# Kernel optimization log

Measured on AMD Instinct MI355X. Metric: run time of the kernel, lower is better.

The kernel has to match this reference:

```python
import jax, jax.numpy as jnp
import numpy as np

K = 30  # top-k spatial positions kept per channel


def setup_inputs() -> dict:
    key = jax.random.key(0)
    k1, k2, k3 = jax.random.split(key, 3)
    b, c, h, w = 32, 384, 56, 56
    x = jax.random.normal(k1, (b, c, h, w), dtype=jnp.float32)
    # depthwise conv: torch weight shape (C, 1, 3, 3), bias (C,)
    fan_in = 1 * 3 * 3
    bound = 1.0 / np.sqrt(fan_in)
    weight = jax.random.uniform(k2, (c, 1, 3, 3), dtype=jnp.float32, minval=-bound, maxval=bound)
    bias = jax.random.uniform(k3, (c,), dtype=jnp.float32, minval=-bound, maxval=bound)
    return {"x": x, "weight": weight, "bias": bias}


def reference(x, weight, bias):
    b, c, h, w = x.shape
    # depthwise 3x3 conv, padding=1 (SAME), groups=c
    scores = jax.lax.conv_general_dilated(
        x, weight,
        window_strides=(1, 1),
        padding="SAME",
        feature_group_count=c,
        dimension_numbers=("NCHW", "OIHW", "NCHW"),
    ) + bias[None, :, None, None]
    scores_flat = scores.reshape(b, c, h * w)
    _, topk_idx = jax.lax.top_k(scores_flat, K)  # (b, c, K)
    bi = jnp.arange(b)[:, None, None]
    ci = jnp.arange(c)[None, :, None]
    mask = jnp.zeros((b, c, h * w), dtype=x.dtype).at[bi, ci, topk_idx].set(1.0)
    return x * mask.reshape(b, c, h, w)
```

## Files before the change

### kernel.cpp

```cpp
#include <hip/hip_runtime.h>

#define NT 256
#define W 56
#define HW 3136
#define PW 60
#define GUARD 64
#define PAD_SZ (GUARD + 58*PW)
#define KSEL 30
#define NQ (HW/4)
#define CAP 160
#define ACT 196

typedef float v2f __attribute__((ext_vector_type(2)));

__device__ __forceinline__ v2f vfma(v2f a, v2f b, v2f c) {
#if __has_builtin(__builtin_elementwise_fma)
    return __builtin_elementwise_fma(a, b, c);
#else
    v2f r; r.x = fmaf(a.x, b.x, c.x); r.y = fmaf(a.y, b.y, c.y); return r;
#endif
}

__global__ __launch_bounds__(NT, 8) void topk_spatial_kernel(
    const float* __restrict__ x,
    const float* __restrict__ wgt,
    const float* __restrict__ bias,
    float* __restrict__ out,
    int C)
{
    __shared__ float        xs[PAD_SZ];
    __shared__ unsigned int smax[NT];
    __shared__ int          c_idx[CAP];
    __shared__ double       c_sd[CAP];
    __shared__ unsigned int keepw[HW / 32];
    __shared__ unsigned int s_T16;
    __shared__ int s_cnt;

    const int tid = threadIdx.x;
    const int bc  = blockIdx.x;
    const int ci  = bc % C;

    const float* xp = x   + (size_t)bc * HW;
    float*       op = out + (size_t)bc * HW;

    const float* wpt = wgt + (size_t)ci * 9;
    const float wk[3][3] = { { wpt[0], wpt[1], wpt[2] },
                             { wpt[3], wpt[4], wpt[5] },
                             { wpt[6], wpt[7], wpt[8] } };
    const float bv = bias[ci];

    if (tid < GUARD) xs[tid] = 0.0f;
    if (tid < PW) {
        xs[GUARD + tid] = 0.0f;
        xs[GUARD + 57 * PW + tid] = 0.0f;
    }
    if (tid < 224) {
        const int rr = 1 + (tid >> 2);
        xs[GUARD + rr * PW + 56 + (tid & 3)] = 0.0f;
    }
    if (tid < HW / 32) keepw[tid] = 0u;
    if (tid == 255) s_cnt = 0;

    for (int t = tid; t < NQ; t += NT) {
        const float4 v = reinterpret_cast<const float4*>(xp)[t];
        const int y = t / 14;
        const int m = t - 14 * y;
        *reinterpret_cast<float4*>(&xs[GUARD + (y + 1) * PW + 4 * m]) = v;
    }
    __syncthreads();

    const bool active = (tid < ACT);
    const int  m_ = tid % 14;
    const int  g_ = tid / 14;

    unsigned int k32[16];
    float4 xm[4];
    unsigned int mx = 0u;

    if (active) {
        v2f accL[4], accH[4];
        #pragma unroll
        for (int k = 0; k < 4; ++k) { accL[k] = v2f{bv, bv}; accH[k] = v2f{bv, bv}; }

        const int base0 = GUARD + (4 * g_) * PW + 4 * m_;
        #pragma unroll
        for (int dr = 0; dr < 6; ++dr) {
            const int b = base0 + dr * PW;
            const float2 vl = *reinterpret_cast<const float2*>(&xs[b - 2]);
            const float4 vm = *reinterpret_cast<const float4*>(&xs[b]);
            const float  vr = xs[b + 4];
            const v2f p0 = { vl.y, vm.x };
            const v2f p1 = { vm.x, vm.y };
            const v2f p2 = { vm.y, vm.z };
            const v2f p3 = { vm.z, vm.w };
            const v2f p4 = { vm.w, vr   };
            #pragma unroll
            for (int k = 0; k < 4; ++k) {
                const int kr = dr - k;
                if (kr >= 0 && kr < 3) {
                    const v2f wA = { wk[kr][0], wk[kr][0] };
                    const v2f wB = { wk[kr][1], wk[kr][1] };
                    const v2f wC = { wk[kr][2], wk[kr][2] };
                    accL[k] = vfma(wA, p0, accL[k]);
                    accL[k] = vfma(wB, p1, accL[k]);
                    accL[k] = vfma(wC, p2, accL[k]);
                    accH[k] = vfma(wA, p2, accH[k]);
                    accH[k] = vfma(wB, p3, accH[k]);
                    accH[k] = vfma(wC, p4, accH[k]);
                }
            }
            if (dr >= 1 && dr <= 4) xm[dr - 1] = vm;
        }

        #pragma unroll
        for (int k = 0; k < 4; ++k) {
            const float sv[4] = { accL[k].x, accL[k].y, accH[k].x, accH[k].y };
            #pragma unroll
            for (int j = 0; j < 4; ++j) {
                const unsigned int bb = __float_as_uint(sv[j]);
                const unsigned int key = ((int)bb < 0) ? ~bb : (bb | 0x80000000u);
                k32[k * 4 + j] = key;
                mx = (key > mx) ? key : mx;
            }
        }
    } else {
        #pragma unroll
        for (int kk = 0; kk < 16; ++kk) k32[kk] = 0u;
    }

    smax[tid] = mx;
    __syncthreads();

    if (tid < 64) {
        const unsigned int m0 = smax[tid]       >> 16;
        const unsigned int m1 = smax[tid + 64]  >> 16;
        const unsigned int m2 = smax[tid + 128] >> 16;
        const unsigned int m3 = smax[tid + 192] >> 16;
        unsigned int lo = 0u, hi = 65536u;
        while (hi - lo > 1u) {
            const unsigned int mid = (lo + hi) >> 1;
            const int c = (m0 >= mid) + (m1 >= mid) + (m2 >= mid) + (m3 >= mid);
            const unsigned long long b0 = __ballot(c & 1);
            const unsigned long long b1 = __ballot(c & 2);
            const unsigned long long b2 = __ballot(c & 4);
            const int cnt = __popcll(b0) + 2 * __popcll(b1) + 4 * __popcll(b2);
            if (cnt >= KSEL) { lo = mid; if (cnt <= 48) break; }
            else hi = mid;
        }
        if (tid == 0) s_T16 = lo;
    }
    __syncthreads();

    const unsigned int binkey = s_T16 << 16;
    const float Tf = (binkey & 0x80000000u)
                         ? __uint_as_float(binkey ^ 0x80000000u)
                         : __uint_as_float(~binkey);
    const float Tm = Tf - 1e-4f;
    const unsigned int tb    = __float_as_uint(Tm);
    const unsigned int TmKey = ((int)tb < 0) ? ~tb : (tb | 0x80000000u);

    if (active) {
        #pragma unroll
        for (int kk = 0; kk < 16; ++kk) {
            if (k32[kk] >= TmKey) {
                const int slot = atomicAdd(&s_cnt, 1);
                if (slot < CAP)
                    c_idx[slot] = (4 * g_ + (kk >> 2)) * W + 4 * m_ + (kk & 3);
            }
        }
    }
    __syncthreads();

    const int E = (s_cnt < CAP) ? s_cnt : CAP;
    if (tid < E) {
        const int i = c_idx[tid];
        const int y = i / W;
        const int p = GUARD + (y + 1) * PW + (i - y * W);
        double s = (double)bv;
        s = fma((double)wk[0][0], (double)xs[p - PW - 1], s);
        s = fma((double)wk[0][1], (double)xs[p - PW    ], s);
        s = fma((double)wk[0][2], (double)xs[p - PW + 1], s);
        s = fma((double)wk[1][0], (double)xs[p - 1],      s);
        s = fma((double)wk[1][1], (double)xs[p],          s);
        s = fma((double)wk[1][2], (double)xs[p + 1],      s);
        s = fma((double)wk[2][0], (double)xs[p + PW - 1], s);
        s = fma((double)wk[2][1], (double)xs[p + PW    ], s);
        s = fma((double)wk[2][2], (double)xs[p + PW + 1], s);
        c_sd[tid] = s;
    }
    __syncthreads();

    if (tid < E) {
        const double se = c_sd[tid];
        const int    ei = c_idx[tid];
        int rank = 0;
        for (int j = 0; j < E; ++j) {
            const double sj = c_sd[j];
            const int    ji = c_idx[j];
            rank += (sj > se) || (sj == se && ji < ei);
        }
        if (rank < KSEL) atomicOr(&keepw[ei >> 5], 1u << (ei & 31));
    }
    __syncthreads();

    if (active) {
        #pragma unroll
        for (int k = 0; k < 4; ++k) {
            const int ib = (4 * g_ + k) * W + 4 * m_;
            const unsigned int bits = keepw[ib >> 5] >> (ib & 31);
            float4 v = xm[k];
            v.x = (bits & 1u) ? v.x : 0.0f;
            v.y = (bits & 2u) ? v.y : 0.0f;
            v.z = (bits & 4u) ? v.z : 0.0f;
            v.w = (bits & 8u) ? v.w : 0.0f;
            *reinterpret_cast<float4*>(&op[ib]) = v;
        }
    }
}

extern "C" void kernel_launch(void* const* d_in, const int* in_sizes, int n_in,
                              void* d_out, int out_size, void* d_ws, size_t ws_size,
                              hipStream_t stream) {
    const float* x  = (const float*)d_in[0];
    const float* w  = (const float*)d_in[1];
    const float* b  = (const float*)d_in[2];
    float* out      = (float*)d_out;

    const int C  = in_sizes[2];
    const int BC = in_sizes[0] / HW;

    topk_spatial_kernel<<<BC, NT, 0, stream>>>(x, w, b, out, C);
}
```

Before: 96.76 us.

## Drop LDS staging of input tile; read conv halos from global with lane shuffles

Removes the padded shared-memory copy of the 56x56 plane and its barrier. Each thread now loads its float4 rows straight from global memory and gets left and right neighbours through wavefront shuffles, using a 16-lane-per-row thread mapping. Candidate rescoring and the final masked store reload x from global (expected to hit L2/L1) instead of shared memory or registers. This cuts LDS footprint, which may raise occupancy, and drops the staging pass. The cost is more global loads and a 16-wide layout that leaves some threads idle.

```diff
diff --git a/kernel.cpp b/kernel.cpp
--- a/kernel.cpp
+++ b/kernel.cpp
@@ -3,13 +3,8 @@
 #define NT 256
 #define W 56
 #define HW 3136
-#define PW 60
-#define GUARD 64
-#define PAD_SZ (GUARD + 58*PW)
 #define KSEL 30
-#define NQ (HW/4)
 #define CAP 160
-#define ACT 196
 
 typedef float v2f __attribute__((ext_vector_type(2)));
 
@@ -28,7 +23,6 @@
     float* __restrict__ out,
     int C)
 {
-    __shared__ float        xs[PAD_SZ];
     __shared__ unsigned int smax[NT];
     __shared__ int          c_idx[CAP];
     __shared__ double       c_sd[CAP];
@@ -49,47 +43,39 @@
                              { wpt[6], wpt[7], wpt[8] } };
     const float bv = bias[ci];
 
-    if (tid < GUARD) xs[tid] = 0.0f;
-    if (tid < PW) {
-        xs[GUARD + tid] = 0.0f;
-        xs[GUARD + 57 * PW + tid] = 0.0f;
-    }
-    if (tid < 224) {
-        const int rr = 1 + (tid >> 2);
-        xs[GUARD + rr * PW + 56 + (tid & 3)] = 0.0f;
-    }
     if (tid < HW / 32) keepw[tid] = 0u;
     if (tid == 255) s_cnt = 0;
 
-    for (int t = tid; t < NQ; t += NT) {
-        const float4 v = reinterpret_cast<const float4*>(xp)[t];
-        const int y = t / 14;
-        const int m = t - 14 * y;
-        *reinterpret_cast<float4*>(&xs[GUARD + (y + 1) * PW + 4 * m]) = v;
-    }
-    __syncthreads();
-
-    const bool active = (tid < ACT);
-    const int  m_ = tid % 14;
-    const int  g_ = tid / 14;
+    const int m_ = tid & 15;
+    const int g_ = tid >> 4;
+    const bool active = (m_ < 14) && (g_ < 14);
+    const int mq = (m_ < 14) ? m_ : 13;
+    const int gq = (g_ < 14) ? g_ : 13;
 
     unsigned int k32[16];
-    float4 xm[4];
     unsigned int mx = 0u;
-
-    if (active) {
+    {
         v2f accL[4], accH[4];
         #pragma unroll
         for (int k = 0; k < 4; ++k) { accL[k] = v2f{bv, bv}; accH[k] = v2f{bv, bv}; }
 
-        const int base0 = GUARD + (4 * g_) * PW + 4 * m_;
+        const int cb = 4 * mq;
         #pragma unroll
         for (int dr = 0; dr < 6; ++dr) {
-            const int b = base0 + dr * PW;
-            const float2 vl = *reinterpret_cast<const float2*>(&xs[b - 2]);
-            const float4 vm = *reinterpret_cast<const float4*>(&xs[b]);
-            const float  vr = xs[b + 4];
-            const v2f p0 = { vl.y, vm.x };
+            const int rr = 4 * gq - 1 + dr;
+            const int ra = (rr < 0) ? 0 : ((rr > 55) ? 55 : rr);
+            const bool rok = (rr >= 0) && (rr < 56);
+            float4 vm = *reinterpret_cast<const float4*>(xp + ra * W + cb);
+            vm.x = rok ? vm.x : 0.0f;
+            vm.y = rok ? vm.y : 0.0f;
+            vm.z = rok ? vm.z : 0.0f;
+            vm.w = rok ? vm.w : 0.0f;
+            const float lraw = __shfl_up(vm.w, 1);
+            const float rraw = __shfl_down(vm.x, 1);
+            const float vl = (m_ == 0)  ? 0.0f : lraw;
+            const float vr = (m_ == 13) ? 0.0f : rraw;
+
+            const v2f p0 = { vl,   vm.x };
             const v2f p1 = { vm.x, vm.y };
             const v2f p2 = { vm.y, vm.z };
             const v2f p3 = { vm.z, vm.w };
@@ -109,23 +95,24 @@
                     accH[k] = vfma(wC, p4, accH[k]);
                 }
             }
-            if (dr >= 1 && dr <= 4) xm[dr - 1] = vm;
-        }
-
-        #pragma unroll
-        for (int k = 0; k < 4; ++k) {
-            const float sv[4] = { accL[k].x, accL[k].y, accH[k].x, accH[k].y };
-            #pragma unroll
-            for (int j = 0; j < 4; ++j) {
-                const unsigned int bb = __float_as_uint(sv[j]);
-                const unsigned int key = ((int)bb < 0) ? ~bb : (bb | 0x80000000u);
-                k32[k * 4 + j] = key;
-                mx = (key > mx) ? key : mx;
-            }
-        }
-    } else {
-        #pragma unroll
-        for (int kk = 0; kk < 16; ++kk) k32[kk] = 0u;
+        }
+
+        if (active) {
+            #pragma unroll
+            for (int k = 0; k < 4; ++k) {
+                const float sv[4] = { accL[k].x, accL[k].y, accH[k].x, accH[k].y };
+                #pragma unroll
+                for (int j = 0; j < 4; ++j) {
+                    const unsigned int bb = __float_as_uint(sv[j]);
+                    const unsigned int key = ((int)bb < 0) ? ~bb : (bb | 0x80000000u);
+                    k32[k * 4 + j] = key;
+                    mx = (key > mx) ? key : mx;
+                }
+            }
+        } else {
+            #pragma unroll
+            for (int kk = 0; kk < 16; ++kk) k32[kk] = 0u;
+        }
     }
 
     smax[tid] = mx;
@@ -173,19 +160,22 @@
 
     const int E = (s_cnt < CAP) ? s_cnt : CAP;
     if (tid < E) {
-        const int i = c_idx[tid];
-        const int y = i / W;
-        const int p = GUARD + (y + 1) * PW + (i - y * W);
+        const int i  = c_idx[tid];
+        const int y  = i / W;
+        const int xc = i - y * W;
         double s = (double)bv;
-        s = fma((double)wk[0][0], (double)xs[p - PW - 1], s);
-        s = fma((double)wk[0][1], (double)xs[p - PW    ], s);
-        s = fma((double)wk[0][2], (double)xs[p - PW + 1], s);
-        s = fma((double)wk[1][0], (double)xs[p - 1],      s);
-        s = fma((double)wk[1][1], (double)xs[p],          s);
-        s = fma((double)wk[1][2], (double)xs[p + 1],      s);
-        s = fma((double)wk[2][0], (double)xs[p + PW - 1], s);
-        s = fma((double)wk[2][1], (double)xs[p + PW    ], s);
-        s = fma((double)wk[2][2], (double)xs[p + PW + 1], s);
+        #pragma unroll
+        for (int dy = -1; dy <= 1; ++dy) {
+            #pragma unroll
+            for (int dx = -1; dx <= 1; ++dx) {
+                const int yy = y + dy, xx = xc + dx;
+                const int ya = (yy < 0) ? 0 : ((yy > 55) ? 55 : yy);
+                const int xa = (xx < 0) ? 0 : ((xx > 55) ? 55 : xx);
+                const float xv = xp[ya * W + xa];
+                const bool ok = ((unsigned)yy < 56u) && ((unsigned)xx < 56u);
+                s = fma((double)wk[dy + 1][dx + 1], ok ? (double)xv : 0.0, s);
+            }
+        }
         c_sd[tid] = s;
     }
     __syncthreads();
@@ -207,8 +197,8 @@
         #pragma unroll
         for (int k = 0; k < 4; ++k) {
             const int ib = (4 * g_ + k) * W + 4 * m_;
+            float4 v = *reinterpret_cast<const float4*>(xp + ib);
             const unsigned int bits = keepw[ib >> 5] >> (ib & 31);
-            float4 v = xm[k];
             v.x = (bits & 1u) ? v.x : 0.0f;
             v.y = (bits & 2u) ? v.y : 0.0f;
             v.z = (bits & 4u) ? v.z : 0.0f;
```

After: 99.64 us. 3.0% more time.
